# Performance work log

Measured on AMD Instinct MI355X. Metric: run time of the kernel, lower is better.

Reference implementation:

```python
import jax, jax.numpy as jnp
import numpy as np

B, Z, D, V, IN, R = 4, 128, 2, 2, 512, 256


def setup_inputs() -> dict:
    key = jax.random.key(0)
    ks = jax.random.split(key, 9)
    scale = 1.0 / np.sqrt(IN)
    inp = {
        "x1": jax.random.normal(ks[0], (B, Z, D, V, IN), jnp.float32),
        "x2": jax.random.normal(ks[1], (B, Z, D, V, IN), jnp.float32),
        "x3": jax.random.normal(ks[2], (B, Z, D, V, IN), jnp.float32),
        "W1": jax.random.normal(ks[3], (IN, R), jnp.float32) * scale,
        "b1": jax.random.normal(ks[4], (R,), jnp.float32) * scale,
        "W2": jax.random.normal(ks[5], (IN, R), jnp.float32) * scale,
        "b2": jax.random.normal(ks[6], (R,), jnp.float32) * scale,
        "W3": jax.random.normal(ks[7], (IN, R), jnp.float32) * scale,
        "b3": jax.random.normal(ks[8], (R,), jnp.float32) * scale,
    }
    return inp


def reference(x1, x2, x3, W1, b1, W2, b2, W3, b3):
    # Linear projections: [b, pos, d, v, in] @ [in, r] -> [b, pos, d, v, r]
    p1 = jnp.einsum('bzdvi,ir->bzdvr', x1, W1) + b1
    p2 = jnp.einsum('bxdvi,ir->bxdvr', x2, W2) + b2
    p3 = jnp.einsum('bcdvi,ir->bcdvr', x3, W3) + b3
    # Trilinear contraction over the factorized rank r, broadcasting over d, v
    return jnp.einsum('bzdve,bxdve,bcdve->bzxcdv', p1, p2, p3)
```

## Files before the change

kernel.cpp:

```cpp
#include <hip/hip_runtime.h>
#include <hip/hip_bf16.h>


typedef _Float16 f16;
typedef __attribute__((ext_vector_type(8)))  _Float16 f16x8;
typedef __attribute__((ext_vector_type(4)))  float    f32x4;
typedef __attribute__((ext_vector_type(16))) float    f32x16;

__device__ __forceinline__ void lds_barrier() {
    __builtin_amdgcn_sched_barrier(0);
    asm volatile("s_waitcnt lgkmcnt(0)" ::: "memory");
    __builtin_amdgcn_s_barrier();
    __builtin_amdgcn_sched_barrier(0);
}

__global__ __launch_bounds__(128) void proj_kernel(
    const float* __restrict__ x1, const float* __restrict__ x2, const float* __restrict__ x3,
    const float* __restrict__ W1, const float* __restrict__ b1,
    const float* __restrict__ W2, const float* __restrict__ b2,
    const float* __restrict__ W3, const float* __restrict__ b3,
    f16* __restrict__ p1, f16* __restrict__ p2, f16* __restrict__ p3) {
    const int mat = blockIdx.z;
    const float* __restrict__ x    = (mat == 0) ? x1 : (mat == 1) ? x2 : x3;
    const float* __restrict__ W    = (mat == 0) ? W1 : (mat == 1) ? W2 : W3;
    const float* __restrict__ bias = (mat == 0) ? b1 : (mat == 1) ? b2 : b3;
    f16* __restrict__ p = (mat == 0) ? p1 : (mat == 1) ? p2 : p3;

    const int tid  = threadIdx.x;
    const int lane = tid & 63;
    const int w    = tid >> 6;
    const int ln   = lane & 31;
    const int kq   = lane >> 5;
    const int m0   = blockIdx.x * 64 + w * 32;
    const int n0b  = blockIdx.y * 32;

    __shared__ f16 sWt[2][32 * 40];

    f32x16 acc;
#pragma unroll
    for (int i = 0; i < 16; ++i) acc[i] = 0.f;

    const int snn = tid & 31, skk0 = tid >> 5;
    const float* Xr = x + (size_t)(m0 + ln) * 512 + kq * 8;

    float wr[8], wr2[8];
    f32x4 xr[4], xn[4];
#pragma unroll
    for (int j = 0; j < 8; ++j)
        wr[j] = W[(size_t)(skk0 + 4 * j) * 256 + n0b + snn];
#pragma unroll
    for (int t = 0; t < 2; ++t) {
        xr[2 * t]     = *(const f32x4*)(Xr + t * 16);
        xr[2 * t + 1] = *(const f32x4*)(Xr + t * 16 + 4);
    }

#pragma unroll 1
    for (int ch = 0; ch < 16; ++ch) {
        const int buf = ch & 1;
#pragma unroll
        for (int j = 0; j < 8; ++j)
            sWt[buf][snn * 40 + skk0 + 4 * j] = (f16)wr[j];
        if (ch < 15) {
            const int k1 = (ch + 1) * 32;
#pragma unroll
            for (int j = 0; j < 8; ++j)
                wr2[j] = W[(size_t)(k1 + skk0 + 4 * j) * 256 + n0b + snn];
#pragma unroll
            for (int t = 0; t < 2; ++t) {
                xn[2 * t]     = *(const f32x4*)(Xr + k1 + t * 16);
                xn[2 * t + 1] = *(const f32x4*)(Xr + k1 + t * 16 + 4);
            }
        }
        lds_barrier();
#pragma unroll
        for (int ks = 0; ks < 2; ++ks) {
            f32x4 a0 = xr[2 * ks], a1 = xr[2 * ks + 1];
            f16x8 av;
            av[0] = (f16)a0[0]; av[1] = (f16)a0[1]; av[2] = (f16)a0[2]; av[3] = (f16)a0[3];
            av[4] = (f16)a1[0]; av[5] = (f16)a1[1]; av[6] = (f16)a1[2]; av[7] = (f16)a1[3];
            f16x8 bv = *(const f16x8*)&sWt[buf][ln * 40 + ks * 16 + kq * 8];
            acc = __builtin_amdgcn_mfma_f32_32x32x16_f16(av, bv, acc, 0, 0, 0);
        }
#pragma unroll
        for (int t = 0; t < 4; ++t) xr[t] = xn[t];
#pragma unroll
        for (int j = 0; j < 8; ++j) wr[j] = wr2[j];
    }

    const int n = n0b + ln;
    const float bn = bias[n];
#pragma unroll
    for (int i = 0; i < 16; ++i) {
        const int m  = m0 + (i & 3) + 8 * (i >> 2) + 4 * kq;
        const int bb = m >> 9, z = (m >> 2) & 127, dv = m & 3;
        p[((bb * 4 + dv) * 128 + z) * 256 + n] = (f16)(acc[i] + bn);
    }
}

__global__ __launch_bounds__(256, 2) void tri_kernel(
    const f16* __restrict__ p1, const f16* __restrict__ p2,
    const f16* __restrict__ p3, float* __restrict__ out) {
    const int bi = blockIdx.x;
    const int zg = bi & 7;
    const int ct = (bi >> 3) & 3;
    const int xt = (bi >> 5) & 3;
    const int b  = bi >> 7;

    const int tid  = threadIdx.x;
    const int lane = tid & 63;
    const int w    = tid >> 6;
    const int ln   = lane & 31;
    const int kq   = lane >> 5;
    const int x0   = xt * 32;
    const int c0   = ct * 32;
    const int z0   = zg * 16;
    const int sl   = b * 4 + w;

    __shared__ __align__(16) f16  sP1[4][16 * 256];
    __shared__ float sT[2][4 * 32 * 33];

#pragma unroll
    for (int i = 0; i < 8; ++i) {
        const int G  = i * 64 + lane;
        const int zo = G >> 5, es = G & 31;
        f16x8 v = *(const f16x8*)(p1 + ((sl * 128 + z0 + zo) << 8) + es * 8);
        *(f16x8*)&sP1[w][G * 8] = v;
    }

    f16x8 pv[16], bq[16];
    const f16* P2r = p2 + ((sl * 128 + x0 + ln) << 8) + kq * 8;
    const f16* P3r = p3 + ((sl * 128 + c0 + ln) << 8) + kq * 8;
#pragma unroll
    for (int ks = 0; ks < 16; ++ks) {
        pv[ks] = *(const f16x8*)(P2r + ks * 16);
        bq[ks] = *(const f16x8*)(P3r + ks * 16);
    }

    const int cl = tid & 31, xg = tid >> 5;

#pragma unroll 1
    for (int zi = 0; zi < 16; ++zi) {
        f32x16 acc;
#pragma unroll
        for (int i = 0; i < 16; ++i) acc[i] = 0.f;

#pragma unroll
        for (int ks = 0; ks < 16; ++ks) {
            f16x8 u = *(const f16x8*)&sP1[w][(zi * 32 + ks * 2 + kq) * 8];
            f16x8 af = u * pv[ks];
            acc = __builtin_amdgcn_mfma_f32_32x32x16_f16(af, bq[ks], acc, 0, 0, 0);
        }

        float* T = sT[zi & 1];
#pragma unroll
        for (int i = 0; i < 16; ++i) {
            const int xl = (i & 3) + 8 * (i >> 2) + 4 * kq;
            T[w * 1056 + xl * 33 + ln] = acc[i];
        }
        lds_barrier();

        const int z = z0 + zi;
#pragma unroll
        for (int j = 0; j < 4; ++j) {
            const int xl = xg * 4 + j;
            f32x4 v;
            v[0] = T[0 * 1056 + xl * 33 + cl];
            v[1] = T[1 * 1056 + xl * 33 + cl];
            v[2] = T[2 * 1056 + xl * 33 + cl];
            v[3] = T[3 * 1056 + xl * 33 + cl];
            const size_t idx = (size_t)((b * 128 + z) * 128 + x0 + xl) * 128 + c0 + cl;
            *(f32x4*)(out + idx * 4) = v;
        }
    }
}

extern "C" void kernel_launch(void* const* d_in, const int* in_sizes, int n_in,
                              void* d_out, int out_size, void* d_ws, size_t ws_size,
                              hipStream_t stream) {
    const float* x1 = (const float*)d_in[0];
    const float* x2 = (const float*)d_in[1];
    const float* x3 = (const float*)d_in[2];
    const float* W1 = (const float*)d_in[3];
    const float* b1 = (const float*)d_in[4];
    const float* W2 = (const float*)d_in[5];
    const float* b2 = (const float*)d_in[6];
    const float* W3 = (const float*)d_in[7];
    const float* b3 = (const float*)d_in[8];

    char* ws = (char*)d_ws;
    f16* p1 = (f16*)ws;
    f16* p2 = (f16*)(ws + (1u << 20));
    f16* p3 = (f16*)(ws + 2u * (1u << 20));

    proj_kernel<<<dim3(32, 8, 3), 128, 0, stream>>>(x1, x2, x3, W1, b1, W2, b2, W3, b3,
                                                    p1, p2, p3);
    tri_kernel<<<dim3(512), 256, 0, stream>>>(p1, p2, p3, (float*)d_out);
}
```

Measured before the change: 51.57 us.

## Widen tri_kernel blocks to two c-tiles sharing one staged p1 tile

The trilinear kernel now runs 512-thread blocks covering a 64-wide c range. Eight waves split into four (d,v) slices times two c halves, and the p1 tile in LDS is loaded once and shared by both halves. Stores become 64 contiguous c values per row, giving longer coalesced output writes. The grid drops to 256 blocks and LDS per block roughly doubles, which lowers occupancy and how many blocks each CU can hold. An extra barrier after the p1 staging is also added.

```diff
diff --git a/kernel.cpp b/kernel.cpp
--- a/kernel.cpp
+++ b/kernel.cpp
@@ -97,46 +97,54 @@
     }
 }
 
-__global__ __launch_bounds__(256, 2) void tri_kernel(
+__global__ __launch_bounds__(512) void tri_kernel(
     const f16* __restrict__ p1, const f16* __restrict__ p2,
     const f16* __restrict__ p3, float* __restrict__ out) {
     const int bi = blockIdx.x;
     const int zg = bi & 7;
-    const int ct = (bi >> 3) & 3;
-    const int xt = (bi >> 5) & 3;
-    const int b  = bi >> 7;
+    const int ct = (bi >> 3) & 1;
+    const int xt = (bi >> 4) & 3;
+    const int b  = bi >> 6;
 
     const int tid  = threadIdx.x;
     const int lane = tid & 63;
     const int w    = tid >> 6;
+    const int dv   = w & 3;
+    const int ct2  = w >> 2;
     const int ln   = lane & 31;
     const int kq   = lane >> 5;
     const int x0   = xt * 32;
-    const int c0   = ct * 32;
+    const int c0w  = ct * 64 + ct2 * 32;
+    const int c0b  = ct * 64;
     const int z0   = zg * 16;
-    const int sl   = b * 4 + w;
+    const int sl   = b * 4 + dv;
 
     __shared__ __align__(16) f16  sP1[4][16 * 256];
-    __shared__ float sT[2][4 * 32 * 33];
-
-#pragma unroll
-    for (int i = 0; i < 8; ++i) {
-        const int G  = i * 64 + lane;
-        const int zo = G >> 5, es = G & 31;
-        f16x8 v = *(const f16x8*)(p1 + ((sl * 128 + z0 + zo) << 8) + es * 8);
-        *(f16x8*)&sP1[w][G * 8] = v;
+    __shared__ float sT[2][4 * 32 * 66];
+
+    if (ct2 == 0) {
+#pragma unroll
+        for (int i = 0; i < 8; ++i) {
+            const int G  = i * 64 + lane;
+            const int zo = G >> 5, es = G & 31;
+            f16x8 v = *(const f16x8*)(p1 + ((sl * 128 + z0 + zo) << 8) + es * 8);
+            *(f16x8*)&sP1[dv][G * 8] = v;
+        }
     }
 
     f16x8 pv[16], bq[16];
     const f16* P2r = p2 + ((sl * 128 + x0 + ln) << 8) + kq * 8;
-    const f16* P3r = p3 + ((sl * 128 + c0 + ln) << 8) + kq * 8;
+    const f16* P3r = p3 + ((sl * 128 + c0w + ln) << 8) + kq * 8;
 #pragma unroll
     for (int ks = 0; ks < 16; ++ks) {
         pv[ks] = *(const f16x8*)(P2r + ks * 16);
         bq[ks] = *(const f16x8*)(P3r + ks * 16);
     }
 
-    const int cl = tid & 31, xg = tid >> 5;
+    lds_barrier();
+
+    const int cl = lane;
+    const int xg = w;
 
 #pragma unroll 1
     for (int zi = 0; zi < 16; ++zi) {
@@ -146,7 +154,7 @@
 
 #pragma unroll
         for (int ks = 0; ks < 16; ++ks) {
-            f16x8 u = *(const f16x8*)&sP1[w][(zi * 32 + ks * 2 + kq) * 8];
+            f16x8 u = *(const f16x8*)&sP1[dv][(zi * 32 + ks * 2 + kq) * 8];
             f16x8 af = u * pv[ks];
             acc = __builtin_amdgcn_mfma_f32_32x32x16_f16(af, bq[ks], acc, 0, 0, 0);
         }
@@ -155,7 +163,7 @@
 #pragma unroll
         for (int i = 0; i < 16; ++i) {
             const int xl = (i & 3) + 8 * (i >> 2) + 4 * kq;
-            T[w * 1056 + xl * 33 + ln] = acc[i];
+            T[(dv * 32 + xl) * 66 + ct2 * 32 + ln] = acc[i];
         }
         lds_barrier();
 
@@ -164,11 +172,11 @@
         for (int j = 0; j < 4; ++j) {
             const int xl = xg * 4 + j;
             f32x4 v;
-            v[0] = T[0 * 1056 + xl * 33 + cl];
-            v[1] = T[1 * 1056 + xl * 33 + cl];
-            v[2] = T[2 * 1056 + xl * 33 + cl];
-            v[3] = T[3 * 1056 + xl * 33 + cl];
-            const size_t idx = (size_t)((b * 128 + z) * 128 + x0 + xl) * 128 + c0 + cl;
+            v[0] = T[(0 * 32 + xl) * 66 + cl];
+            v[1] = T[(1 * 32 + xl) * 66 + cl];
+            v[2] = T[(2 * 32 + xl) * 66 + cl];
+            v[3] = T[(3 * 32 + xl) * 66 + cl];
+            const size_t idx = (size_t)((b * 128 + z) * 128 + x0 + xl) * 128 + c0b + cl;
             *(f32x4*)(out + idx * 4) = v;
         }
     }
@@ -194,5 +202,5 @@
 
     proj_kernel<<<dim3(32, 8, 3), 128, 0, stream>>>(x1, x2, x3, W1, b1, W2, b2, W3, b3,
                                                     p1, p2, p3);
-    tri_kernel<<<dim3(512), 256, 0, stream>>>(p1, p2, p3, (float*)d_out);
-}
+    tri_kernel<<<dim3(256), 512, 0, stream>>>(p1, p2, p3, (float*)d_out);
+}
```

New measurement: 53.58 us. 3.9% more time.
